# Performance work log

Measured on AMD Instinct MI355X. Metric: run time of the kernel, lower is better.

Reference implementation:

```python
import jax, jax.numpy as jnp
import numpy as np

B, N, NFEAT, NHID, NOUT = 16, 2048, 128, 128, 64
BN_EPS = 1e-5
LRELU_ALPHA = 0.2


def setup_inputs() -> dict:
    key = jax.random.key(0)
    ks = jax.random.split(key, 6)
    stdv = 1.0 / np.sqrt(NHID)
    return {
        "x": jax.random.normal(ks[0], (B, N, NFEAT), dtype=jnp.float32),
        "adj": jnp.zeros((N, N), dtype=jnp.float32),  # passed to GAT but unused
        "adj_gcn": jax.random.uniform(ks[1], (N, N), dtype=jnp.float32),
        "gcn_weight": jax.random.uniform(ks[2], (NFEAT, NHID), minval=-stdv, maxval=stdv, dtype=jnp.float32),
        "gcn_bias": jax.random.uniform(ks[3], (NHID,), minval=-stdv, maxval=stdv, dtype=jnp.float32),
        "bn_gamma": jnp.ones((NHID,), dtype=jnp.float32),
        "bn_beta": jnp.zeros((NHID,), dtype=jnp.float32),
        "gat_W": jax.random.normal(ks[4], (NFEAT, NOUT), dtype=jnp.float32) * 0.05,
    }


def reference(x, adj, adj_gcn, gcn_weight, gcn_bias, bn_gamma, bn_beta, gat_W):
    # --- GCN layer: adj @ (x @ W) + b ---
    support = jnp.einsum("bnc,cd->bnd", x, gcn_weight)
    h = jnp.einsum("nm,bmd->bnd", adj_gcn, support) + gcn_bias  # [B,N,nhid]
    # --- BatchNorm1d (training mode: batch stats over B,N per channel) ---
    mean = h.mean(axis=(0, 1))
    var = h.var(axis=(0, 1))
    h = (h - mean) * jax.lax.rsqrt(var + BN_EPS) * bn_gamma + bn_beta
    # --- ReLU ---
    h = jax.nn.relu(h)
    # --- GAT layer (adj arg unused, as in original) ---
    h_prime = jnp.einsum("bnd,de->bne", h, gat_W)  # [B,N,nout]
    e = jnp.einsum("bne,bme->bnm", h_prime, h_prime)  # [B,N,N]
    e = jnp.where(e > 0, e, LRELU_ALPHA * e)  # LeakyReLU(0.2)
    attention = jax.nn.softmax(e, axis=1)  # softmax over dim=1 (as in source)
    # repeat-mul-sum over dim=2 reduces exactly to row-sum scaling of h_prime
    out = h_prime * attention.sum(axis=2, keepdims=True)  # [B,N,nout]
    return out
```

## Files before the change

### kernel.cpp

```cpp
#include <hip/hip_runtime.h>
#include <math.h>

#define NB 16
#define NN 2048
#define NF 128
#define NH 128
#define NO 64

typedef short bf16x8 __attribute__((ext_vector_type(8)));
typedef float f32x4 __attribute__((ext_vector_type(4)));
typedef unsigned short u16;
typedef unsigned int u32;

#define LOG2E 1.4426950408889634f
#define EXPSHIFT 43.28085122666891f

__device__ __forceinline__ u16 f2bf(float f) {
  u32 u = __builtin_bit_cast(u32, f);
  return (u16)((u + 0x7fffu + ((u >> 16) & 1u)) >> 16);
}
__device__ __forceinline__ float bf2f(u16 h) {
  u32 u = ((u32)h) << 16;
  return __builtin_bit_cast(float, u);
}

__device__ __forceinline__ void gload16(const void* g, void* l) {
  __builtin_amdgcn_global_load_lds((const __attribute__((address_space(1))) void*)g,
                                   (__attribute__((address_space(3))) void*)l, 16, 0, 0);
}
__device__ __forceinline__ f32x4 mfma16(bf16x8 a, bf16x8 b, f32x4 c) {
  return __builtin_amdgcn_mfma_f32_16x16x32_bf16(a, b, c, 0, 0, 0);
}
__device__ __forceinline__ float explr(float z) {
  return __builtin_amdgcn_exp2f(fmaf(fmaxf(z, 0.2f * z), LOG2E, -EXPSHIFT));
}

__global__ __launch_bounds__(256) void k_prep(const float* __restrict__ x,
                                              const float* __restrict__ adj,
                                              const float* __restrict__ gcn_w,
                                              const float* __restrict__ gat_w,
                                              u16* __restrict__ x_sw,
                                              u16* __restrict__ adj_sw,
                                              u16* __restrict__ Wg_sw,
                                              u16* __restrict__ Wsw) {
  __shared__ u16 ts[128 * 136];
  const int t = threadIdx.x;
  const int bid = blockIdx.x;
  if (bid == 0) {
#pragma unroll
    for (int it = 0; it < 4; ++it) {
      const int s = t + it * 256;
      const int kb = s >> 6, col = s & 63;
      u16 tmp[8];
#pragma unroll
      for (int j = 0; j < 8; ++j) tmp[j] = f2bf(gat_w[(kb * 8 + j) * 64 + col]);
      uint4 o;
      o.x = (u32)tmp[0] | ((u32)tmp[1] << 16);
      o.y = (u32)tmp[2] | ((u32)tmp[3] << 16);
      o.z = (u32)tmp[4] | ((u32)tmp[5] << 16);
      o.w = (u32)tmp[6] | ((u32)tmp[7] << 16);
      *(uint4*)&Wg_sw[(size_t)s * 8] = o;
    }
  } else if (bid < 9) {
    const int s = (bid - 1) * 256 + t;
    const int kb = s >> 7, d = s & 127;
    u16 tmp[8];
#pragma unroll
    for (int j = 0; j < 8; ++j) tmp[j] = f2bf(gcn_w[(kb * 8 + j) * 128 + d]);
    uint4 o;
    o.x = (u32)tmp[0] | ((u32)tmp[1] << 16);
    o.y = (u32)tmp[2] | ((u32)tmp[3] << 16);
    o.z = (u32)tmp[4] | ((u32)tmp[5] << 16);
    o.w = (u32)tmp[6] | ((u32)tmp[7] << 16);
    *(uint4*)&Wsw[(size_t)s * 8] = o;
  } else if (bid < 265) {
    const int blk = bid - 9;
    const size_t r0 = (size_t)blk * 128;
#pragma unroll
    for (int k = 0; k < 16; ++k) {
      const int s = t + k * 256;
      const int row = s >> 5, c4 = (s & 31) * 4;
      const float4 f = *(const float4*)&x[(r0 + row) * 128 + c4];
      uint2 pk;
      pk.x = (u32)f2bf(f.x) | ((u32)f2bf(f.y) << 16);
      pk.y = (u32)f2bf(f.z) | ((u32)f2bf(f.w) << 16);
      *(uint2*)&ts[row * 136 + c4] = pk;
    }
    __syncthreads();
#pragma unroll
    for (int k = 0; k < 8; ++k) {
      const int s = t + k * 256;
      const int kb = s >> 7, row = s & 127;
      const uint4 v = *(const uint4*)&ts[row * 136 + kb * 8];
      *(uint4*)&x_sw[(size_t)blk * 16384 + (size_t)s * 8] = v;
    }
  } else {
    const int tile = bid - 265;
    const int n0 = (tile >> 5) * 64, m0 = (tile & 31) * 64;
#pragma unroll
    for (int k = 0; k < 4; ++k) {
      const int s = t + k * 256;
      const int row = s >> 4, c4 = (s & 15) * 4;
      const float4 f = *(const float4*)&adj[(size_t)(n0 + row) * 2048 + m0 + c4];
      uint2 pk;
      pk.x = (u32)f2bf(f.x) | ((u32)f2bf(f.y) << 16);
      pk.y = (u32)f2bf(f.z) | ((u32)f2bf(f.w) << 16);
      *(uint2*)&ts[row * 136 + c4] = pk;
    }
    __syncthreads();
#pragma unroll
    for (int k = 0; k < 2; ++k) {
      const int s = t + k * 256;
      const int kb = s >> 6, row = s & 63;
      const uint4 v = *(const uint4*)&ts[row * 136 + kb * 8];
      *(uint4*)&adj_sw[(size_t)tile * 4096 + (size_t)s * 8] = v;
    }
  }
}

__global__ __launch_bounds__(256) void k_support(const u16* __restrict__ x_sw,
                                                 const u16* __restrict__ Wsw,
                                                 u16* __restrict__ suppT_sw) {
  const int m0g = blockIdx.x * 128;
  const int t = threadIdx.x, w = t >> 6, l = t & 63;
  const int lg = l >> 4, lr = l & 15;
  __shared__ __align__(16) u16 sh[32768];
  u16* As = sh;
  u16* Bs = sh + 16384;
#pragma unroll
  for (int i = 0; i < 8; ++i) {
    const int s0 = i * 256 + w * 64;
    gload16(x_sw + (size_t)blockIdx.x * 16384 + (size_t)(s0 + l) * 8, &As[(size_t)s0 * 8]);
  }
#pragma unroll
  for (int i = 0; i < 8; ++i) {
    const int s0 = i * 256 + w * 64;
    gload16(Wsw + (size_t)(s0 + l) * 8, &Bs[(size_t)s0 * 8]);
  }
  __syncthreads();
  f32x4 acc[2][8];
#pragma unroll
  for (int mf = 0; mf < 2; ++mf)
#pragma unroll
    for (int nf = 0; nf < 8; ++nf) {
      acc[mf][nf][0] = 0.f; acc[mf][nf][1] = 0.f;
      acc[mf][nf][2] = 0.f; acc[mf][nf][3] = 0.f;
    }
#pragma unroll
  for (int ks = 0; ks < 4; ++ks) {
    const int kb = ks * 4 + lg;
    const bf16x8 a0 = *(const bf16x8*)&As[((size_t)kb * 128 + w * 32 + lr) * 8];
    const bf16x8 a1 = *(const bf16x8*)&As[((size_t)kb * 128 + w * 32 + 16 + lr) * 8];
#pragma unroll
    for (int nf = 0; nf < 8; ++nf) {
      const bf16x8 b = *(const bf16x8*)&Bs[((size_t)kb * 128 + nf * 16 + lr) * 8];
      acc[0][nf] = mfma16(a0, b, acc[0][nf]);
      acc[1][nf] = mfma16(a1, b, acc[1][nf]);
    }
  }
  __syncthreads();
  u16* os = sh;
#pragma unroll
  for (int nf = 0; nf < 8; ++nf) {
    const int d = nf * 16 + lr;
#pragma unroll
    for (int mf = 0; mf < 2; ++mf) {
      const int mb = w * 32 + mf * 16 + lg * 4;
      const u32 p0 = (u32)f2bf(acc[mf][nf][0]) | ((u32)f2bf(acc[mf][nf][1]) << 16);
      const u32 p1 = (u32)f2bf(acc[mf][nf][2]) | ((u32)f2bf(acc[mf][nf][3]) << 16);
      *(u32*)&os[d * 136 + mb] = p0;
      *(u32*)&os[d * 136 + mb + 2] = p1;
    }
  }
  __syncthreads();
  const int b = m0g >> 11, mt0 = (m0g & 2047) >> 6;
#pragma unroll
  for (int i = 0; i < 8; ++i) {
    const int s = i * 256 + t;
    const int kt = s >> 10, kb = (s >> 7) & 7, d = s & 127;
    const uint4 v = *(const uint4*)&os[d * 136 + kt * 64 + kb * 8];
    *(uint4*)&suppT_sw[((size_t)((b * 32 + mt0 + kt) * 8 + kb)) * 1024 + (size_t)d * 8] = v;
  }
}

__global__ __launch_bounds__(512) void k_gcn(const u16* __restrict__ adj_sw,
                                             const u16* __restrict__ suppT_sw,
                                             const float* __restrict__ bias,
                                             float* __restrict__ h,
                                             float* __restrict__ psum,
                                             float* __restrict__ psq) {
  const int nt = blockIdx.x;
  const int b = blockIdx.y;
  const int n0 = nt * 64;
  const int t = threadIdx.x;
  const int w = t >> 6, l = t & 63;
  const int wm = w >> 1, wn = w & 1;
  const int lg = l >> 4, lr = l & 15;
  __shared__ __align__(16) u16 As[2][4096];
  __shared__ __align__(16) u16 Bs[2][8192];
  __shared__ float redS[4][128], redQ[4][128];

  f32x4 acc[4];
#pragma unroll
  for (int nf = 0; nf < 4; ++nf) {
    acc[nf][0] = 0.f; acc[nf][1] = 0.f;
    acc[nf][2] = 0.f; acc[nf][3] = 0.f;
  }

#define GCN_STAGE(buf, kt)                                                        \
  {                                                                               \
    gload16(adj_sw + ((size_t)(nt * 32 + (kt))) * 4096 + (size_t)t * 8,           \
            &As[buf][t * 8]);                                                     \
    _Pragma("unroll") for (int i = 0; i < 2; ++i) {                               \
      const int s = i * 512 + t;                                                  \
      gload16(suppT_sw + ((size_t)(b * 32 + (kt))) * 8192 + (size_t)s * 8,        \
              &Bs[buf][s * 8]);                                                   \
    }                                                                             \
  }

  GCN_STAGE(0, 0);
  __syncthreads();
  for (int kt = 0; kt < 32; ++kt) {
    const int cur = kt & 1;
    if (kt + 1 < 32) GCN_STAGE(cur ^ 1, kt + 1);
#pragma unroll
    for (int kb = 0; kb < 2; ++kb) {
      const int ko = kb * 4 + lg;
      const bf16x8 a0 = *(const bf16x8*)&As[cur][(ko * 64 + wm * 16 + lr) * 8];
      const bf16x8 b0 = *(const bf16x8*)&Bs[cur][(ko * 128 + wn * 64 + lr) * 8];
      const bf16x8 b1 = *(const bf16x8*)&Bs[cur][(ko * 128 + wn * 64 + 16 + lr) * 8];
      const bf16x8 b2 = *(const bf16x8*)&Bs[cur][(ko * 128 + wn * 64 + 32 + lr) * 8];
      const bf16x8 b3 = *(const bf16x8*)&Bs[cur][(ko * 128 + wn * 64 + 48 + lr) * 8];
      acc[0] = mfma16(a0, b0, acc[0]);
      acc[1] = mfma16(a0, b1, acc[1]);
      acc[2] = mfma16(a0, b2, acc[2]);
      acc[3] = mfma16(a0, b3, acc[3]);
    }
    __syncthreads();
  }
#undef GCN_STAGE
#pragma unroll
  for (int nf = 0; nf < 4; ++nf) {
    const int d = wn * 64 + nf * 16 + lr;
    const float bv = bias[d];
    float s = 0.f, q = 0.f;
#pragma unroll
    for (int r = 0; r < 4; ++r) {
      const float v = acc[nf][r] + bv;
      const int row = n0 + wm * 16 + lg * 4 + r;
      h[((size_t)(b * NN + row)) * NH + d] = v;
      s += v;
      q = fmaf(v, v, q);
    }
    s += __shfl_xor(s, 16);
    s += __shfl_xor(s, 32);
    q += __shfl_xor(q, 16);
    q += __shfl_xor(q, 32);
    if (lg == 0) {
      redS[wm][d] = s;
      redQ[wm][d] = q;
    }
  }
  __syncthreads();
  if (t < 128) {
    const int blk = b * 32 + nt;
    psum[blk * 128 + t] = redS[0][t] + redS[1][t] + redS[2][t] + redS[3][t];
    psq[blk * 128 + t] = redQ[0][t] + redQ[1][t] + redQ[2][t] + redQ[3][t];
  }
}

__global__ __launch_bounds__(1024) void k_bnstat2(const float* __restrict__ psum,
                                                  const float* __restrict__ psq,
                                                  const float* __restrict__ gamma,
                                                  const float* __restrict__ beta,
                                                  float* __restrict__ scale,
                                                  float* __restrict__ shift) {
  const int t = threadIdx.x;
  const int d = t & 127;
  const int g = t >> 7;
  float s = 0.f, q = 0.f;
  for (int i = g; i < 512; i += 8) {
    s += psum[i * 128 + d];
    q += psq[i * 128 + d];
  }
  __shared__ float ls[8][128], lq[8][128];
  ls[g][d] = s;
  lq[g][d] = q;
  __syncthreads();
  if (t < 128) {
    s = 0.f;
    q = 0.f;
#pragma unroll
    for (int i = 0; i < 8; ++i) {
      s += ls[i][t];
      q += lq[i][t];
    }
    const float inv = 1.f / (float)(NB * NN);
    const float mean = s * inv;
    const float var = q * inv - mean * mean;
    const float sc = gamma[t] * rsqrtf(var + 1e-5f);
    scale[t] = sc;
    shift[t] = beta[t] - mean * sc;
  }
}

__global__ __launch_bounds__(256) void k_hp(const float* __restrict__ h,
                                            const float* __restrict__ scale,
                                            const float* __restrict__ shift,
                                            const u16* __restrict__ Wg_sw,
                                            u16* __restrict__ hp_sw) {
  const int row0 = blockIdx.x * 64;
  const int t = threadIdx.x, w = t >> 6, l = t & 63;
  const int lg = l >> 4, lr = l & 15;
  __shared__ __align__(16) u16 him[8192];
  __shared__ __align__(16) u16 Wg[8192];
  __shared__ __align__(16) u16 hos[64][72];
  __shared__ float scs[128], shs[128];
#pragma unroll
  for (int i = 0; i < 4; ++i) {
    const int s0 = i * 256 + w * 64;
    gload16(Wg_sw + (size_t)(s0 + l) * 8, &Wg[(size_t)s0 * 8]);
  }
  if (t < 128) {
    scs[t] = scale[t];
    shs[t] = shift[t];
  }
  __syncthreads();
#pragma unroll
  for (int k = 0; k < 4; ++k) {
    const int s = t + k * 256;
    const int row = s >> 4, kb = s & 15;
    const float4 v0 = *(const float4*)&h[(size_t)(row0 + row) * NH + kb * 8];
    const float4 v1 = *(const float4*)&h[(size_t)(row0 + row) * NH + kb * 8 + 4];
    u16 p[8];
    p[0] = f2bf(fmaxf(fmaf(v0.x, scs[kb * 8 + 0], shs[kb * 8 + 0]), 0.f));
    p[1] = f2bf(fmaxf(fmaf(v0.y, scs[kb * 8 + 1], shs[kb * 8 + 1]), 0.f));
    p[2] = f2bf(fmaxf(fmaf(v0.z, scs[kb * 8 + 2], shs[kb * 8 + 2]), 0.f));
    p[3] = f2bf(fmaxf(fmaf(v0.w, scs[kb * 8 + 3], shs[kb * 8 + 3]), 0.f));
    p[4] = f2bf(fmaxf(fmaf(v1.x, scs[kb * 8 + 4], shs[kb * 8 + 4]), 0.f));
    p[5] = f2bf(fmaxf(fmaf(v1.y, scs[kb * 8 + 5], shs[kb * 8 + 5]), 0.f));
    p[6] = f2bf(fmaxf(fmaf(v1.z, scs[kb * 8 + 6], shs[kb * 8 + 6]), 0.f));
    p[7] = f2bf(fmaxf(fmaf(v1.w, scs[kb * 8 + 7], shs[kb * 8 + 7]), 0.f));
    uint4 o;
    o.x = (u32)p[0] | ((u32)p[1] << 16);
    o.y = (u32)p[2] | ((u32)p[3] << 16);
    o.z = (u32)p[4] | ((u32)p[5] << 16);
    o.w = (u32)p[6] | ((u32)p[7] << 16);
    const int boff = (row * 256 + kb * 16) ^ ((row & 7) << 4);
    *(uint4*)&him[boff >> 1] = o;
  }
  __syncthreads();
  f32x4 acc[4];
#pragma unroll
  for (int nf = 0; nf < 4; ++nf) {
    acc[nf][0] = 0.f; acc[nf][1] = 0.f;
    acc[nf][2] = 0.f; acc[nf][3] = 0.f;
  }
#pragma unroll
  for (int kks = 0; kks < 4; ++kks) {
    const int ko = kks * 4 + lg;
    const int arow = w * 16 + lr;
    const int aoff = (arow * 256 + ko * 16) ^ ((arow & 7) << 4);
    const bf16x8 a = *(const bf16x8*)&him[aoff >> 1];
#pragma unroll
    for (int nf = 0; nf < 4; ++nf) {
      const bf16x8 bfr = *(const bf16x8*)&Wg[(ko * 64 + nf * 16 + lr) * 8];
      acc[nf] = mfma16(a, bfr, acc[nf]);
    }
  }
#pragma unroll
  for (int nf = 0; nf < 4; ++nf) {
    const int col = nf * 16 + lr;
#pragma unroll
    for (int r = 0; r < 4; ++r) {
      hos[w * 16 + lg * 4 + r][col] = f2bf(acc[nf][r]);
    }
  }
  __syncthreads();
  const size_t tbase = (size_t)blockIdx.x * 4096;
#pragma unroll
  for (int k = 0; k < 2; ++k) {
    const int s = t + k * 256;
    const int kb = s >> 6, r6 = s & 63;
    const uint2 lo = *(const uint2*)&hos[r6][kb * 8];
    const uint2 hi = *(const uint2*)&hos[r6][kb * 8 + 4];
    uint4 o;
    o.x = lo.x; o.y = lo.y; o.z = hi.x; o.w = hi.y;
    *(uint4*)&hp_sw[tbase + kb * 512 + r6 * 8] = o;
  }
}

__global__ __launch_bounds__(256) void k_attnA(const u16* __restrict__ hp_sw,
                                               float* __restrict__ Dpart) {
  const int bx = blockIdx.x, qtr = blockIdx.y;
  const int b = bx >> 5, nt = bx & 31;
  const int t = threadIdx.x, w = t >> 6, l = t & 63;
  const int lg = l >> 4, lr = l & 15;
  __shared__ __align__(16) u16 Cs[2][4096];
  const u16* rbase = hp_sw + (size_t)(b * 32 + nt) * 4096;
  const int qrow = (w << 4) + lr;
  const bf16x8 bq0 = *(const bf16x8*)&rbase[(lg * 64 + qrow) * 8];
  const bf16x8 bq1 = *(const bf16x8*)&rbase[((lg + 4) * 64 + qrow) * 8];
  const u16* cb = hp_sw + (size_t)(b * 32 + qtr * 8) * 4096;
#pragma unroll
  for (int i = 0; i < 2; ++i) gload16(cb + (size_t)(i * 256 + t) * 8, &Cs[0][(i * 256 + t) * 8]);
  __syncthreads();
  float S = 0.f;
  for (int mt = 0; mt < 8; ++mt) {
    const int cur = mt & 1;
    if (mt + 1 < 8) {
#pragma unroll
      for (int i = 0; i < 2; ++i)
        gload16(cb + (size_t)(mt + 1) * 4096 + (size_t)(i * 256 + t) * 8,
                &Cs[cur ^ 1][(i * 256 + t) * 8]);
    }
#pragma unroll
    for (int mf = 0; mf < 4; ++mf) {
      const bf16x8 a0 = *(const bf16x8*)&Cs[cur][(lg * 64 + mf * 16 + lr) * 8];
      const bf16x8 a1 = *(const bf16x8*)&Cs[cur][((lg + 4) * 64 + mf * 16 + lr) * 8];
      f32x4 z;
      z[0] = 0.f; z[1] = 0.f; z[2] = 0.f; z[3] = 0.f;
      z = mfma16(a0, bq0, z);
      z = mfma16(a1, bq1, z);
      S += explr(z[0]) + explr(z[1]) + explr(z[2]) + explr(z[3]);
    }
    __syncthreads();
  }
  S += __shfl_xor(S, 16);
  S += __shfl_xor(S, 32);
  if (l < 16) Dpart[qtr * 32768 + b * NN + nt * 64 + qrow] = S;
}

__global__ __launch_bounds__(256) void k_attnB(const u16* __restrict__ hp_sw,
                                               const float* __restrict__ Dpart,
                                               float* __restrict__ Spart) {
  const int bx = blockIdx.x, qtr = blockIdx.y;
  const int b = bx >> 5, nt = bx & 31;
  const int t = threadIdx.x, w = t >> 6, l = t & 63;
  const int lg = l >> 4, lr = l & 15;
  __shared__ __align__(16) u16 Cs[2][4096];
  __shared__ float iDs[512];
  const u16* rbase = hp_sw + (size_t)(b * 32 + nt) * 4096;
  const int qrow = (w << 4) + lr;
  const bf16x8 bq0 = *(const bf16x8*)&rbase[(lg * 64 + qrow) * 8];
  const bf16x8 bq1 = *(const bf16x8*)&rbase[((lg + 4) * 64 + qrow) * 8];
  const u16* cb = hp_sw + (size_t)(b * 32 + qtr * 8) * 4096;
#pragma unroll
  for (int i = 0; i < 2; ++i) gload16(cb + (size_t)(i * 256 + t) * 8, &Cs[0][(i * 256 + t) * 8]);
#pragma unroll
  for (int i = 0; i < 2; ++i) {
    const int idx = t + i * 256;
    const int n = b * NN + qtr * 512 + idx;
    iDs[idx] = 1.f / (Dpart[n] + Dpart[32768 + n] + Dpart[65536 + n] + Dpart[98304 + n]);
  }
  __syncthreads();
  float S = 0.f;
  for (int mt = 0; mt < 8; ++mt) {
    const int cur = mt & 1;
    if (mt + 1 < 8) {
#pragma unroll
      for (int i = 0; i < 2; ++i)
        gload16(cb + (size_t)(mt + 1) * 4096 + (size_t)(i * 256 + t) * 8,
                &Cs[cur ^ 1][(i * 256 + t) * 8]);
    }
#pragma unroll
    for (int mf = 0; mf < 4; ++mf) {
      const bf16x8 a0 = *(const bf16x8*)&Cs[cur][(lg * 64 + mf * 16 + lr) * 8];
      const bf16x8 a1 = *(const bf16x8*)&Cs[cur][((lg + 4) * 64 + mf * 16 + lr) * 8];
      f32x4 z;
      z[0] = 0.f; z[1] = 0.f; z[2] = 0.f; z[3] = 0.f;
      z = mfma16(a0, bq0, z);
      z = mfma16(a1, bq1, z);
      const float4 dv = *(const float4*)&iDs[mt * 64 + mf * 16 + lg * 4];
      S = fmaf(explr(z[0]), dv.x, S);
      S = fmaf(explr(z[1]), dv.y, S);
      S = fmaf(explr(z[2]), dv.z, S);
      S = fmaf(explr(z[3]), dv.w, S);
    }
    __syncthreads();
  }
  S += __shfl_xor(S, 16);
  S += __shfl_xor(S, 32);
  if (l < 16) Spart[qtr * 32768 + b * NN + nt * 64 + qrow] = S;
}

__global__ __launch_bounds__(256) void k_scale(const u16* __restrict__ hp_sw,
                                               const float* __restrict__ Spart,
                                               float* __restrict__ out) {
  const int bx = blockIdx.x;
  const int b = bx >> 5, nt = bx & 31;
  const int t = threadIdx.x;
  __shared__ float Sv[64];
  if (t < 64) {
    const int n = b * NN + nt * 64 + t;
    Sv[t] = Spart[n] + Spart[32768 + n] + Spart[65536 + n] + Spart[98304 + n];
  }
  __syncthreads();
  const u16* rbase = hp_sw + (size_t)(b * 32 + nt) * 4096;
  const int row = t >> 2;
  const float sc = Sv[row];
  const size_t R = (size_t)b * NN + nt * 64 + row;
#pragma unroll
  for (int hh = 0; hh < 2; ++hh) {
    const int kb = (t & 3) * 2 + hh;
    const u16* src = &rbase[(kb * 64 + row) * 8];
    float4 o0, o1;
    o0.x = bf2f(src[0]) * sc;
    o0.y = bf2f(src[1]) * sc;
    o0.z = bf2f(src[2]) * sc;
    o0.w = bf2f(src[3]) * sc;
    o1.x = bf2f(src[4]) * sc;
    o1.y = bf2f(src[5]) * sc;
    o1.z = bf2f(src[6]) * sc;
    o1.w = bf2f(src[7]) * sc;
    *(float4*)&out[R * NO + kb * 8] = o0;
    *(float4*)&out[R * NO + kb * 8 + 4] = o1;
  }
}

extern "C" void kernel_launch(void* const* d_in, const int* in_sizes, int n_in,
                              void* d_out, int out_size, void* d_ws, size_t ws_size,
                              hipStream_t stream) {
  const float* x = (const float*)d_in[0];
  const float* adj_gcn = (const float*)d_in[2];
  const float* gcn_w = (const float*)d_in[3];
  const float* gcn_b = (const float*)d_in[4];
  const float* gamma = (const float*)d_in[5];
  const float* beta = (const float*)d_in[6];
  const float* gat_w = (const float*)d_in[7];
  float* out = (float*)d_out;
  float* ws = (float*)d_ws;

  u16* adj_sw = (u16*)ws;
  u16* suppT_sw = (u16*)(ws + 2097152);
  float* hbuf = ws + 4194304;
  u16* x_sw = (u16*)(ws + 4194304);
  u16* hp_sw = (u16*)(ws + 8388608);
  float* psum = ws + 9437184;
  float* psq = psum + 65536;
  float* scale = psq + 65536;
  float* shift = scale + 128;
  u16* Wg_sw = (u16*)(shift + 128);
  u16* Wsw = (u16*)(shift + 128 + 4096);
  float* Dpart = ws + 9617664;
  float* Spart = Dpart + 131072;

  k_prep<<<dim3(1289), dim3(256), 0, stream>>>(x, adj_gcn, gcn_w, gat_w, x_sw, adj_sw, Wg_sw, Wsw);
  k_support<<<dim3(256), dim3(256), 0, stream>>>(x_sw, Wsw, suppT_sw);
  k_gcn<<<dim3(32, 16), dim3(512), 0, stream>>>(adj_sw, suppT_sw, gcn_b, hbuf, psum, psq);
  k_bnstat2<<<dim3(1), dim3(1024), 0, stream>>>(psum, psq, gamma, beta, scale, shift);
  k_hp<<<dim3(512), dim3(256), 0, stream>>>(hbuf, scale, shift, Wg_sw, hp_sw);
  k_attnA<<<dim3(512, 4), dim3(256), 0, stream>>>(hp_sw, Dpart);
  k_attnB<<<dim3(512, 4), dim3(256), 0, stream>>>(hp_sw, Dpart, Spart);
  k_scale<<<dim3(512), dim3(256), 0, stream>>>(hp_sw, Spart, out);
}
```

Before: 115.9 us.

## Fuse x bf16 conversion into support GEMM and swizzle block order for L2 locality

Removes the x fp32-to-bf16 pre-swizzle pass from k_prep. k_support now loads fp32 x directly, converts it to bf16 and stores it into padded LDS before the MFMA loop, which avoids writing and re-reading the x_sw intermediate in global memory. Separately, k_gcn and the two attention kernels remap their block indices so that consecutive dispatched blocks are spread across batches, aiming to balance L2/XCD locality of shared operands. The remap could instead hurt cache reuse if neighbouring blocks previously shared data.

```diff
diff --git a/kernel.cpp b/kernel.cpp
--- a/kernel.cpp
+++ b/kernel.cpp
@@ -35,15 +35,13 @@
   return __builtin_amdgcn_exp2f(fmaf(fmaxf(z, 0.2f * z), LOG2E, -EXPSHIFT));
 }
 
-__global__ __launch_bounds__(256) void k_prep(const float* __restrict__ x,
-                                              const float* __restrict__ adj,
+__global__ __launch_bounds__(256) void k_prep(const float* __restrict__ adj,
                                               const float* __restrict__ gcn_w,
                                               const float* __restrict__ gat_w,
-                                              u16* __restrict__ x_sw,
                                               u16* __restrict__ adj_sw,
                                               u16* __restrict__ Wg_sw,
                                               u16* __restrict__ Wsw) {
-  __shared__ u16 ts[128 * 136];
+  __shared__ u16 ts[64 * 136];
   const int t = threadIdx.x;
   const int bid = blockIdx.x;
   if (bid == 0) {
@@ -73,29 +71,8 @@
     o.z = (u32)tmp[4] | ((u32)tmp[5] << 16);
     o.w = (u32)tmp[6] | ((u32)tmp[7] << 16);
     *(uint4*)&Wsw[(size_t)s * 8] = o;
-  } else if (bid < 265) {
-    const int blk = bid - 9;
-    const size_t r0 = (size_t)blk * 128;
-#pragma unroll
-    for (int k = 0; k < 16; ++k) {
-      const int s = t + k * 256;
-      const int row = s >> 5, c4 = (s & 31) * 4;
-      const float4 f = *(const float4*)&x[(r0 + row) * 128 + c4];
-      uint2 pk;
-      pk.x = (u32)f2bf(f.x) | ((u32)f2bf(f.y) << 16);
-      pk.y = (u32)f2bf(f.z) | ((u32)f2bf(f.w) << 16);
-      *(uint2*)&ts[row * 136 + c4] = pk;
-    }
-    __syncthreads();
-#pragma unroll
-    for (int k = 0; k < 8; ++k) {
-      const int s = t + k * 256;
-      const int kb = s >> 7, row = s & 127;
-      const uint4 v = *(const uint4*)&ts[row * 136 + kb * 8];
-      *(uint4*)&x_sw[(size_t)blk * 16384 + (size_t)s * 8] = v;
-    }
   } else {
-    const int tile = bid - 265;
+    const int tile = bid - 9;
     const int n0 = (tile >> 5) * 64, m0 = (tile & 31) * 64;
 #pragma unroll
     for (int k = 0; k < 4; ++k) {
@@ -118,25 +95,29 @@
   }
 }
 
-__global__ __launch_bounds__(256) void k_support(const u16* __restrict__ x_sw,
+__global__ __launch_bounds__(256) void k_support(const float* __restrict__ x,
                                                  const u16* __restrict__ Wsw,
                                                  u16* __restrict__ suppT_sw) {
   const int m0g = blockIdx.x * 128;
   const int t = threadIdx.x, w = t >> 6, l = t & 63;
   const int lg = l >> 4, lr = l & 15;
-  __shared__ __align__(16) u16 sh[32768];
-  u16* As = sh;
-  u16* Bs = sh + 16384;
-#pragma unroll
-  for (int i = 0; i < 8; ++i) {
-    const int s0 = i * 256 + w * 64;
-    gload16(x_sw + (size_t)blockIdx.x * 16384 + (size_t)(s0 + l) * 8, &As[(size_t)s0 * 8]);
-  }
+  __shared__ __align__(16) u16 ts[128 * 136];
+  __shared__ __align__(16) u16 Bs[16384];
 #pragma unroll
   for (int i = 0; i < 8; ++i) {
     const int s0 = i * 256 + w * 64;
     gload16(Wsw + (size_t)(s0 + l) * 8, &Bs[(size_t)s0 * 8]);
   }
+#pragma unroll
+  for (int k = 0; k < 16; ++k) {
+    const int s = t + k * 256;
+    const int row = s >> 5, c4 = (s & 31) * 4;
+    const float4 f = *(const float4*)&x[(size_t)(m0g + row) * 128 + c4];
+    uint2 pk;
+    pk.x = (u32)f2bf(f.x) | ((u32)f2bf(f.y) << 16);
+    pk.y = (u32)f2bf(f.z) | ((u32)f2bf(f.w) << 16);
+    *(uint2*)&ts[row * 136 + c4] = pk;
+  }
   __syncthreads();
   f32x4 acc[2][8];
 #pragma unroll
@@ -149,8 +130,8 @@
 #pragma unroll
   for (int ks = 0; ks < 4; ++ks) {
     const int kb = ks * 4 + lg;
-    const bf16x8 a0 = *(const bf16x8*)&As[((size_t)kb * 128 + w * 32 + lr) * 8];
-    const bf16x8 a1 = *(const bf16x8*)&As[((size_t)kb * 128 + w * 32 + 16 + lr) * 8];
+    const bf16x8 a0 = *(const bf16x8*)&ts[(w * 32 + lr) * 136 + kb * 8];
+    const bf16x8 a1 = *(const bf16x8*)&ts[(w * 32 + 16 + lr) * 136 + kb * 8];
 #pragma unroll
     for (int nf = 0; nf < 8; ++nf) {
       const bf16x8 b = *(const bf16x8*)&Bs[((size_t)kb * 128 + nf * 16 + lr) * 8];
@@ -159,7 +140,7 @@
     }
   }
   __syncthreads();
-  u16* os = sh;
+  u16* os = ts;
 #pragma unroll
   for (int nf = 0; nf < 8; ++nf) {
     const int d = nf * 16 + lr;
@@ -189,8 +170,9 @@
                                              float* __restrict__ h,
                                              float* __restrict__ psum,
                                              float* __restrict__ psq) {
-  const int nt = blockIdx.x;
-  const int b = blockIdx.y;
+  const int flat = blockIdx.y * 32 + blockIdx.x;
+  const int nf2 = (flat & 7) * 64 + (flat >> 3);
+  const int b = nf2 >> 5, nt = nf2 & 31;
   const int n0 = nt * 64;
   const int t = threadIdx.x;
   const int w = t >> 6, l = t & 63;
@@ -390,10 +372,19 @@
   }
 }
 
+__device__ __forceinline__ void attn_swz(int& b, int& nt, int& qtr) {
+  const int flat = blockIdx.y * 512 + blockIdx.x;
+  const int lf = (flat & 7) * 256 + (flat >> 3);
+  b = lf >> 7;
+  const int rem = lf & 127;
+  qtr = rem >> 5;
+  nt = rem & 31;
+}
+
 __global__ __launch_bounds__(256) void k_attnA(const u16* __restrict__ hp_sw,
                                                float* __restrict__ Dpart) {
-  const int bx = blockIdx.x, qtr = blockIdx.y;
-  const int b = bx >> 5, nt = bx & 31;
+  int b, nt, qtr;
+  attn_swz(b, nt, qtr);
   const int t = threadIdx.x, w = t >> 6, l = t & 63;
   const int lg = l >> 4, lr = l & 15;
   __shared__ __align__(16) u16 Cs[2][4096];
@@ -434,8 +425,8 @@
 __global__ __launch_bounds__(256) void k_attnB(const u16* __restrict__ hp_sw,
                                                const float* __restrict__ Dpart,
                                                float* __restrict__ Spart) {
-  const int bx = blockIdx.x, qtr = blockIdx.y;
-  const int b = bx >> 5, nt = bx & 31;
+  int b, nt, qtr;
+  attn_swz(b, nt, qtr);
   const int t = threadIdx.x, w = t >> 6, l = t & 63;
   const int lg = l >> 4, lr = l & 15;
   __shared__ __align__(16) u16 Cs[2][4096];
@@ -534,7 +525,6 @@
   u16* adj_sw = (u16*)ws;
   u16* suppT_sw = (u16*)(ws + 2097152);
   float* hbuf = ws + 4194304;
-  u16* x_sw = (u16*)(ws + 4194304);
   u16* hp_sw = (u16*)(ws + 8388608);
   float* psum = ws + 9437184;
   float* psq = psum + 65536;
@@ -545,8 +535,8 @@
   float* Dpart = ws + 9617664;
   float* Spart = Dpart + 131072;
 
-  k_prep<<<dim3(1289), dim3(256), 0, stream>>>(x, adj_gcn, gcn_w, gat_w, x_sw, adj_sw, Wg_sw, Wsw);
-  k_support<<<dim3(256), dim3(256), 0, stream>>>(x_sw, Wsw, suppT_sw);
+  k_prep<<<dim3(1033), dim3(256), 0, stream>>>(adj_gcn, gcn_w, gat_w, adj_sw, Wg_sw, Wsw);
+  k_support<<<dim3(256), dim3(256), 0, stream>>>(x, Wsw, suppT_sw);
   k_gcn<<<dim3(32, 16), dim3(512), 0, stream>>>(adj_sw, suppT_sw, gcn_b, hbuf, psum, psq);
   k_bnstat2<<<dim3(1), dim3(1024), 0, stream>>>(psum, psq, gamma, beta, scale, shift);
   k_hp<<<dim3(512), dim3(256), 0, stream>>>(hbuf, scale, shift, Wg_sw, hp_sw);
```

Measured after the change: 113.0 us. -2.5%, faster.
